# Kernel optimization log

Measured on AMD Instinct MI355X. Metric: run time of the kernel, lower is better.

The kernel has to match this reference:

```python
import jax, jax.numpy as jnp
import numpy as np

B, M, N = 256, 256, 256

def setup_inputs() -> dict:
    key = jax.random.key(0)
    k1, k2 = jax.random.split(key)
    x_real = jax.random.normal(k1, (B, M, N), dtype=jnp.float32)
    x_imag = jax.random.normal(k2, (B, M, N), dtype=jnp.float32)
    return {"x_real": x_real, "x_imag": x_imag}

def reference(x_real, x_imag):
    # complex k-space input; original used complex128 via numpy on host,
    # we use complex64 (the natural accelerator precision), same math.
    x = jax.lax.complex(x_real, x_imag)  # [B, M, N]
    axes = (-2, -1)
    # centered 2D IFFT per sample (ifft_along_dim): fftshift(ifft2(ifftshift(x)))
    y = jnp.fft.fftshift(jnp.fft.ifft2(jnp.fft.ifftshift(x, axes=axes), axes=axes), axes=axes)
    y = y.reshape(-1, 1, M, N)  # (-1, 1, M, N) as in call()
    return (jnp.real(y), jnp.imag(y))
```

## Files before the change

kernel.cpp:

```cpp
#include <hip/hip_runtime.h>
#include <hip/hip_fp16.h>

namespace {

constexpr int NN   = 256;
constexpr int BMN  = 256 * 256 * 256;
constexpr int LPAD = 272;

struct cpx { float re, im; };

__device__ __forceinline__ cpx cadd(cpx a, cpx b){ return cpx{a.re + b.re, a.im + b.im}; }
__device__ __forceinline__ cpx csub(cpx a, cpx b){ return cpx{a.re - b.re, a.im - b.im}; }
__device__ __forceinline__ cpx cmul(cpx a, cpx b){ return cpx{a.re*b.re - a.im*b.im, a.re*b.im + a.im*b.re}; }
__device__ __forceinline__ cpx cmuli(cpx a){ return cpx{-a.im, a.re}; }

__device__ __forceinline__ void r4(cpx a, cpx b, cpx c, cpx d,
                                   cpx& y0, cpx& y1, cpx& y2, cpx& y3) {
  cpx apc = cadd(a, c), amc = csub(a, c);
  cpx bpd = cadd(b, d), bmd = csub(b, d);
  cpx ib  = cmuli(bmd);
  y0 = cadd(apc, bpd);
  y1 = cadd(amc, ib);
  y2 = csub(apc, bpd);
  y3 = csub(amc, ib);
}

__device__ __forceinline__ void ifft16(cpx x[16]) {
  constexpr float WC[10] = { 1.f,  0.9238795325112867f,  0.7071067811865476f,  0.3826834323650898f, 0.f,
                            -0.3826834323650898f, -0.7071067811865476f, -0.9238795325112867f, -1.f,
                            -0.9238795325112867f };
  constexpr float WS[10] = { 0.f,  0.3826834323650898f,  0.7071067811865476f,  0.9238795325112867f, 1.f,
                             0.9238795325112867f,  0.7071067811865476f,  0.3826834323650898f,  0.f,
                            -0.3826834323650898f };
  cpx B[4][4];
#pragma unroll
  for (int n1 = 0; n1 < 4; ++n1)
    r4(x[n1], x[n1 + 4], x[n1 + 8], x[n1 + 12],
       B[n1][0], B[n1][1], B[n1][2], B[n1][3]);
#pragma unroll
  for (int n1 = 1; n1 < 4; ++n1)
#pragma unroll
    for (int k2 = 1; k2 < 4; ++k2)
      B[n1][k2] = cmul(B[n1][k2], cpx{WC[n1 * k2], WS[n1 * k2]});
#pragma unroll
  for (int k2 = 0; k2 < 4; ++k2)
    r4(B[0][k2], B[1][k2], B[2][k2], B[3][k2],
       x[k2], x[k2 + 4], x[k2 + 8], x[k2 + 12]);
}

__device__ __forceinline__ void twiddle256(cpx a[16], int t) {
  const float base = 0.024543692606170259f * (float)t;
#pragma unroll
  for (int k1 = 1; k1 < 16; ++k1) {
    float s, c;
    __sincosf(base * (float)k1, &s, &c);
    a[k1] = cmul(a[k1], cpx{c, s});
  }
}

__global__ __launch_bounds__(256)
void k_ifft_rows(const float* __restrict__ xr, const float* __restrict__ xi,
                 __half* __restrict__ wr, __half* __restrict__ wi) {
  __shared__ float Lr[16 * LPAD];
  __shared__ float Li[16 * LPAD];
  const int tid = threadIdx.x;
  const int t   = tid & 15;
  const int ll  = tid >> 4;

  const size_t blk = (size_t)blockIdx.x * (16 * NN);
  const float4* sr4 = reinterpret_cast<const float4*>(xr + blk);
  const float4* si4 = reinterpret_cast<const float4*>(xi + blk);

#pragma unroll
  for (int q = 0; q < 4; ++q) {
    const int fi   = (q << 8) + tid;
    const int line = fi >> 6;
    const int slot = fi & 63;
    *reinterpret_cast<float4*>(&Lr[line * LPAD + slot * 4]) = sr4[fi];
    *reinterpret_cast<float4*>(&Li[line * LPAD + slot * 4]) = si4[fi];
  }
  __syncthreads();

  cpx a[16];
  {
    const float* lr = Lr + ll * LPAD;
    const float* li = Li + ll * LPAD;
#pragma unroll
    for (int j = 0; j < 16; ++j) {
      const int idx = (((j << 4) | t) ^ 128);
      a[j] = cpx{ lr[idx], li[idx] };
    }
  }
  ifft16(a);
  twiddle256(a, t);
  __syncthreads();

  {
    float* lr = Lr + ll * LPAD;
    float* li = Li + ll * LPAD;
#pragma unroll
    for (int k1 = 0; k1 < 16; ++k1) { lr[k1 * 17 + t] = a[k1].re; li[k1 * 17 + t] = a[k1].im; }
    __syncthreads();
#pragma unroll
    for (int n2 = 0; n2 < 16; ++n2) { a[n2].re = lr[t * 17 + n2]; a[n2].im = li[t * 17 + n2]; }
  }
  ifft16(a);
  __syncthreads();

  {
    float* lr = Lr + ll * LPAD;
    float* li = Li + ll * LPAD;
#pragma unroll
    for (int k = 0; k < 16; ++k) {
      const int idx = (((k << 4) | t) ^ 128);
      lr[idx] = a[k].re;
      li[idx] = a[k].im;
    }
  }
  __syncthreads();

  constexpr float s1 = 1.0f / 256.0f;
  uint2* dr = reinterpret_cast<uint2*>(wr) + (size_t)blockIdx.x * 1024;
  uint2* di = reinterpret_cast<uint2*>(wi) + (size_t)blockIdx.x * 1024;
#pragma unroll
  for (int q = 0; q < 4; ++q) {
    const int fi   = (q << 8) + tid;
    const int line = fi >> 6;
    const int slot = fi & 63;
    const float4 vr = *reinterpret_cast<const float4*>(&Lr[line * LPAD + slot * 4]);
    const float4 vi = *reinterpret_cast<const float4*>(&Li[line * LPAD + slot * 4]);
    union { __half2 h[2]; uint2 u; } pr, pi_;
    pr.h[0]  = __floats2half2_rn(vr.x * s1, vr.y * s1);
    pr.h[1]  = __floats2half2_rn(vr.z * s1, vr.w * s1);
    pi_.h[0] = __floats2half2_rn(vi.x * s1, vi.y * s1);
    pi_.h[1] = __floats2half2_rn(vi.z * s1, vi.w * s1);
    dr[fi] = pr.u;
    di[fi] = pi_.u;
  }
}

__global__ __launch_bounds__(512)
void k_ifft_cols(const __half* __restrict__ wr, const __half* __restrict__ wi,
                 float* __restrict__ yr, float* __restrict__ yi) {
  __shared__ float lbuf[32 * 273];
  const int tid = threadIdx.x;
  const int c   = tid & 31;
  const int t   = tid >> 5;
  const int b   = blockIdx.x >> 3;
  const int c0  = (blockIdx.x & 7) << 5;
  const int base = b * 65536 + c0 + c;

  cpx a[16];
#pragma unroll
  for (int j = 0; j < 16; ++j) {
    const int m = (((j << 4) | t) ^ 128);
    a[j] = cpx{ __half2float(wr[base + m * NN]), __half2float(wi[base + m * NN]) };
  }
  ifft16(a);
  twiddle256(a, t);

  {
    float* L = lbuf + c * 273;
#pragma unroll
    for (int k1 = 0; k1 < 16; ++k1) L[k1 * 17 + t] = a[k1].re;
    __syncthreads();
    float br[16];
#pragma unroll
    for (int n2 = 0; n2 < 16; ++n2) br[n2] = L[t * 17 + n2];
    __syncthreads();
#pragma unroll
    for (int k1 = 0; k1 < 16; ++k1) L[k1 * 17 + t] = a[k1].im;
    __syncthreads();
#pragma unroll
    for (int n2 = 0; n2 < 16; ++n2) { a[n2].im = L[t * 17 + n2]; a[n2].re = br[n2]; }
  }

  ifft16(a);
  constexpr float sc = 1.0f / 256.0f;
#pragma unroll
  for (int k = 0; k < 16; ++k) {
    const int m = (((k << 4) | t) ^ 128);
    __builtin_nontemporal_store(a[k].re * sc, &yr[base + m * NN]);
    __builtin_nontemporal_store(a[k].im * sc, &yi[base + m * NN]);
  }
}

}

extern "C" void kernel_launch(void* const* d_in, const int* in_sizes, int n_in,
                              void* d_out, int out_size, void* d_ws, size_t ws_size,
                              hipStream_t stream) {
  const float* xr = (const float*)d_in[0];
  const float* xi = (const float*)d_in[1];
  float* yr = (float*)d_out;
  float* yi = yr + BMN;
  __half* wr = (__half*)d_ws;
  __half* wi = wr + BMN;

  k_ifft_rows<<<4096, 256, 0, stream>>>(xr, xi, wr, wi);
  k_ifft_cols<<<2048, 512, 0, stream>>>(wr, wi, yr, yi);
}
```

Measured before the change: 79.33 us.

## Split input fp32-to-fp16 conversion into separate kernel before row FFT

```diff
diff --git a/kernel.cpp b/kernel.cpp
--- a/kernel.cpp
+++ b/kernel.cpp
@@ -6,6 +6,8 @@
 constexpr int NN   = 256;
 constexpr int BMN  = 256 * 256 * 256;
 constexpr int LPAD = 272;
+
+typedef float f4 __attribute__((ext_vector_type(4)));
 
 struct cpx { float re, im; };
 
@@ -59,8 +61,30 @@
 }
 
 __global__ __launch_bounds__(256)
-void k_ifft_rows(const float* __restrict__ xr, const float* __restrict__ xi,
-                 __half* __restrict__ wr, __half* __restrict__ wi) {
+void k_convert(const float* __restrict__ xr, const float* __restrict__ xi,
+               __half* __restrict__ wr, __half* __restrict__ wi) {
+  constexpr float s1 = 1.0f / 256.0f;
+  const int n4  = BMN / 4;
+  const int nth = gridDim.x * blockDim.x;
+  const f4* xr4 = reinterpret_cast<const f4*>(xr);
+  const f4* xi4 = reinterpret_cast<const f4*>(xi);
+  uint2* wr2 = reinterpret_cast<uint2*>(wr);
+  uint2* wi2 = reinterpret_cast<uint2*>(wi);
+  for (int g = blockIdx.x * blockDim.x + threadIdx.x; g < n4; g += nth) {
+    const f4 vr = xr4[g];
+    const f4 vi = xi4[g];
+    union { __half2 h[2]; uint2 u; } hr, hi;
+    hr.h[0] = __floats2half2_rn(vr.x * s1, vr.y * s1);
+    hr.h[1] = __floats2half2_rn(vr.z * s1, vr.w * s1);
+    hi.h[0] = __floats2half2_rn(vi.x * s1, vi.y * s1);
+    hi.h[1] = __floats2half2_rn(vi.z * s1, vi.w * s1);
+    wr2[g] = hr.u;
+    wi2[g] = hi.u;
+  }
+}
+
+__global__ __launch_bounds__(256)
+void k_fft_rows(__half* __restrict__ wr, __half* __restrict__ wi) {
   __shared__ float Lr[16 * LPAD];
   __shared__ float Li[16 * LPAD];
   const int tid = threadIdx.x;
@@ -68,16 +92,24 @@
   const int ll  = tid >> 4;
 
   const size_t blk = (size_t)blockIdx.x * (16 * NN);
-  const float4* sr4 = reinterpret_cast<const float4*>(xr + blk);
-  const float4* si4 = reinterpret_cast<const float4*>(xi + blk);
+  uint2* pr = reinterpret_cast<uint2*>(wr + blk);
+  uint2* pi = reinterpret_cast<uint2*>(wi + blk);
 
 #pragma unroll
   for (int q = 0; q < 4; ++q) {
     const int fi   = (q << 8) + tid;
-    const int line = fi >> 6;
-    const int slot = fi & 63;
-    *reinterpret_cast<float4*>(&Lr[line * LPAD + slot * 4]) = sr4[fi];
-    *reinterpret_cast<float4*>(&Li[line * LPAD + slot * 4]) = si4[fi];
+    const int p    = fi << 2;
+    const int line = p >> 8;
+    const int idx  = p & 255;
+    union { uint2 u; __half2 h[2]; } ur, ui;
+    ur.u = pr[fi];
+    ui.u = pi[fi];
+    const float2 r0 = __half22float2(ur.h[0]);
+    const float2 r1 = __half22float2(ur.h[1]);
+    const float2 i0 = __half22float2(ui.h[0]);
+    const float2 i1 = __half22float2(ui.h[1]);
+    *reinterpret_cast<f4*>(&Lr[line * LPAD + idx]) = (f4){r0.x, r0.y, r1.x, r1.y};
+    *reinterpret_cast<f4*>(&Li[line * LPAD + idx]) = (f4){i0.x, i0.y, i1.x, i1.y};
   }
   __syncthreads();
 
@@ -119,23 +151,22 @@
   }
   __syncthreads();
 
-  constexpr float s1 = 1.0f / 256.0f;
-  uint2* dr = reinterpret_cast<uint2*>(wr) + (size_t)blockIdx.x * 1024;
-  uint2* di = reinterpret_cast<uint2*>(wi) + (size_t)blockIdx.x * 1024;
+  constexpr float s2 = 1.0f / 256.0f;
 #pragma unroll
   for (int q = 0; q < 4; ++q) {
     const int fi   = (q << 8) + tid;
-    const int line = fi >> 6;
-    const int slot = fi & 63;
-    const float4 vr = *reinterpret_cast<const float4*>(&Lr[line * LPAD + slot * 4]);
-    const float4 vi = *reinterpret_cast<const float4*>(&Li[line * LPAD + slot * 4]);
-    union { __half2 h[2]; uint2 u; } pr, pi_;
-    pr.h[0]  = __floats2half2_rn(vr.x * s1, vr.y * s1);
-    pr.h[1]  = __floats2half2_rn(vr.z * s1, vr.w * s1);
-    pi_.h[0] = __floats2half2_rn(vi.x * s1, vi.y * s1);
-    pi_.h[1] = __floats2half2_rn(vi.z * s1, vi.w * s1);
-    dr[fi] = pr.u;
-    di[fi] = pi_.u;
+    const int p    = fi << 2;
+    const int line = p >> 8;
+    const int idx  = p & 255;
+    const f4 vr = *reinterpret_cast<const f4*>(&Lr[line * LPAD + idx]);
+    const f4 vi = *reinterpret_cast<const f4*>(&Li[line * LPAD + idx]);
+    union { __half2 h[2]; uint2 u; } hr, hi;
+    hr.h[0] = __floats2half2_rn(vr.x * s2, vr.y * s2);
+    hr.h[1] = __floats2half2_rn(vr.z * s2, vr.w * s2);
+    hi.h[0] = __floats2half2_rn(vi.x * s2, vi.y * s2);
+    hi.h[1] = __floats2half2_rn(vi.z * s2, vi.w * s2);
+    pr[fi] = hr.u;
+    pi[fi] = hi.u;
   }
 }
 
@@ -176,12 +207,11 @@
   }
 
   ifft16(a);
-  constexpr float sc = 1.0f / 256.0f;
 #pragma unroll
   for (int k = 0; k < 16; ++k) {
     const int m = (((k << 4) | t) ^ 128);
-    __builtin_nontemporal_store(a[k].re * sc, &yr[base + m * NN]);
-    __builtin_nontemporal_store(a[k].im * sc, &yi[base + m * NN]);
+    __builtin_nontemporal_store(a[k].re, &yr[base + m * NN]);
+    __builtin_nontemporal_store(a[k].im, &yi[base + m * NN]);
   }
 }
 
@@ -197,6 +227,7 @@
   __half* wr = (__half*)d_ws;
   __half* wi = wr + BMN;
 
-  k_ifft_rows<<<4096, 256, 0, stream>>>(xr, xi, wr, wi);
+  k_convert <<<2048, 256, 0, stream>>>(xr, xi, wr, wi);
+  k_fft_rows<<<4096, 256, 0, stream>>>(wr, wi);
   k_ifft_cols<<<2048, 512, 0, stream>>>(wr, wi, yr, yi);
 }
```

Result: slower. 101.6 us (+28.0%).
